# Performance work log

Hardware: AMD Instinct MI355X
Metric: run time of the kernel (lower is better)

Reference implementation:

```python
import jax, jax.numpy as jnp
import numpy as np

D_MODEL = 512
N_HEADS = 8
N_LAYERS = 2
EPS = 1e-5  # torch LayerNorm default


def _ln(x, w, b):
    m = x.mean(-1, keepdims=True)
    v = ((x - m) ** 2).mean(-1, keepdims=True)
    return (x - m) / jnp.sqrt(v + EPS) * w + b


def _mha(q, k, v, in_w, in_b, out_w, out_b, n_heads, mask=None):
    # matches torch.nn.MultiheadAttention (batch_first, packed in_proj of shape (3D, D))
    D = q.shape[-1]
    hd = D // n_heads
    Q = q @ in_w[:D].T + in_b[:D]
    K = k @ in_w[D:2 * D].T + in_b[D:2 * D]
    V = v @ in_w[2 * D:].T + in_b[2 * D:]
    def heads(t):
        B, T, _ = t.shape
        return t.reshape(B, T, n_heads, hd).transpose(0, 2, 1, 3)
    Qh, Kh, Vh = heads(Q), heads(K), heads(V)
    s = jnp.einsum('bhqd,bhkd->bhqk', Qh, Kh) / np.sqrt(hd).astype(np.float32)
    if mask is not None:
        s = s + mask
    a = jax.nn.softmax(s, axis=-1)
    o = jnp.einsum('bhqk,bhkd->bhqd', a, Vh)
    o = o.transpose(0, 2, 1, 3).reshape(q.shape[0], q.shape[1], D)
    return o @ out_w.T + out_b


def _forward(x, ts, ode_w1, ode_b1, ode_w2, ode_b2,
             gru_wih, gru_whh, gru_bih, gru_bhh, te_a, te_b,
             t_in_w, t_in_b, t_out_w, t_out_b, t_ln1_w, t_ln1_b, t_ln2_w, t_ln2_b,
             t_ff1_w, t_ff1_b, t_ff2_w, t_ff2_b, t_lnf_w, t_lnf_b,
             ca_in_w, ca_in_b, ca_out_w, ca_out_b, ca_lin_w, ca_lin_b, ca_ln_w, ca_ln_b):
    B, T, D = x.shape
    # --- RK4 'jump-ODE' states. In the source, h is overwritten with x[:, i] at the
    # end of every step, so state_i depends only on (x[:,i-1], x[:,i], dt_i):
    # fully parallel over T (no scan needed). ODEFunc assumed: MLP tanh.
    ode = lambda y: jnp.tanh(y @ ode_w1.T + ode_b1) @ ode_w2.T + ode_b2
    dt = (ts[:, 1:] - ts[:, :-1])[..., None]            # (B,T-1,1)
    delta = (x[:, 1:] - x[:, :-1]) / dt                  # (B,T-1,D)
    f1 = ode(delta)
    f2 = ode(delta + 0.5 * dt * f1)
    f3 = ode(delta + 0.5 * dt * f2)
    f4 = ode(delta + dt * f3)
    states = x[:, :-1] + dt / 6.0 * (f1 + 2 * f2 + 2 * f3 + f4)
    H = jnp.concatenate([jnp.zeros((B, 1, D), x.dtype), states], axis=1)
    # --- GRUCell recurrence over T (true dependency -> lax.scan)
    Hd = gru_whh.shape[1]
    gx = H @ gru_wih.T + gru_bih                         # (B,T,3H) precomputed input proj
    def gru_step(h, xg):
        gh = h @ gru_whh.T + gru_bhh
        r = jax.nn.sigmoid(xg[:, :Hd] + gh[:, :Hd])
        zz = jax.nn.sigmoid(xg[:, Hd:2 * Hd] + gh[:, Hd:2 * Hd])
        n = jnp.tanh(xg[:, 2 * Hd:] + r * gh[:, 2 * Hd:])
        h = (1 - zz) * n + zz * h
        return h, h
    _, Hs = jax.lax.scan(gru_step, jnp.zeros((B, Hd), x.dtype), gx.transpose(1, 0, 2))
    H = Hs.transpose(1, 0, 2)                            # (B,T,H)
    # --- TimeHybridEncoding: even channels <- interleaved [sin,cos], odd <- ramp
    n_freq = (D // 2) // 2
    freqs = jnp.exp(-jnp.linspace(0.0, np.log(10000.0 / 4.0), n_freq)) * (2.0 * np.pi / 4.0)
    phase = ts[..., None] * freqs                        # (B,T,n_freq)
    sc = jnp.stack([jnp.sin(phase), jnp.cos(phase)], axis=-1).reshape(B, T, -1)
    ramp = ts[..., None] * te_a + te_b                   # (B,T,D//2)
    tm = jnp.zeros((B, T, D), x.dtype).at[..., 0::2].set(sc).at[..., 1::2].set(ramp)
    z = x + tm
    # --- pre-norm TransformerEncoder with causal mask (relu FFN, final LayerNorm)
    mask = jnp.where(jnp.triu(jnp.ones((T, T), bool), 1), jnp.float32(-1e9), jnp.float32(0.0)).astype(x.dtype)
    for l in range(N_LAYERS):
        y = _ln(z, t_ln1_w[l], t_ln1_b[l])
        z = z + _mha(y, y, y, t_in_w[l], t_in_b[l], t_out_w[l], t_out_b[l], N_HEADS, mask)
        y = _ln(z, t_ln2_w[l], t_ln2_b[l])
        z = z + jax.nn.relu(y @ t_ff1_w[l].T + t_ff1_b[l]) @ t_ff2_w[l].T + t_ff2_b[l]
    z = _ln(z, t_lnf_w, t_lnf_b)
    # --- cross attention: query = GRU states, kv = transformer output
    attn = _mha(H, z, z, ca_in_w, ca_in_b, ca_out_w, ca_out_b, N_HEADS, None)
    H = _ln(H + attn @ ca_lin_w.T + ca_lin_b, ca_ln_w, ca_ln_b)
    return H


def setup_inputs() -> dict:
    key = jax.random.key(0)
    B, T, D, L = 8, 1024, D_MODEL, N_LAYERS
    ks = iter(jax.random.split(key, 48))
    nrm = lambda *s: 0.02 * jax.random.normal(next(ks), s, jnp.float32)
    x = jax.random.normal(next(ks), (B, T, D), jnp.float32)
    # strictly increasing, roughly-normalized timestamps
    ts = jnp.cumsum(jax.random.uniform(next(ks), (B, T), jnp.float32, 0.01, 1.0), axis=1) / T
    return dict(
        x=x, ts=ts,
        ode_w1=nrm(D, D), ode_b1=jnp.zeros((D,), jnp.float32),
        ode_w2=nrm(D, D), ode_b2=jnp.zeros((D,), jnp.float32),
        gru_wih=nrm(3 * D, D), gru_whh=nrm(3 * D, D),
        gru_bih=jnp.zeros((3 * D,), jnp.float32), gru_bhh=jnp.zeros((3 * D,), jnp.float32),
        te_a=nrm(D // 2), te_b=nrm(D // 2),
        t_in_w=nrm(L, 3 * D, D), t_in_b=jnp.zeros((L, 3 * D), jnp.float32),
        t_out_w=nrm(L, D, D), t_out_b=jnp.zeros((L, D), jnp.float32),
        t_ln1_w=jnp.ones((L, D), jnp.float32), t_ln1_b=jnp.zeros((L, D), jnp.float32),
        t_ln2_w=jnp.ones((L, D), jnp.float32), t_ln2_b=jnp.zeros((L, D), jnp.float32),
        t_ff1_w=nrm(L, 4 * D, D), t_ff1_b=jnp.zeros((L, 4 * D), jnp.float32),
        t_ff2_w=nrm(L, D, 4 * D), t_ff2_b=jnp.zeros((L, D), jnp.float32),
        t_lnf_w=jnp.ones((D,), jnp.float32), t_lnf_b=jnp.zeros((D,), jnp.float32),
        ca_in_w=nrm(3 * D, D), ca_in_b=jnp.zeros((3 * D,), jnp.float32),
        ca_out_w=nrm(D, D), ca_out_b=jnp.zeros((D,), jnp.float32),
        ca_lin_w=nrm(D, D), ca_lin_b=jnp.zeros((D,), jnp.float32),
        ca_ln_w=jnp.ones((D,), jnp.float32), ca_ln_b=jnp.zeros((D,), jnp.float32))


def reference(x, ts, ode_w1, ode_b1, ode_w2, ode_b2,
              gru_wih, gru_whh, gru_bih, gru_bhh, te_a, te_b,
              t_in_w, t_in_b, t_out_w, t_out_b, t_ln1_w, t_ln1_b, t_ln2_w, t_ln2_b,
              t_ff1_w, t_ff1_b, t_ff2_w, t_ff2_b, t_lnf_w, t_lnf_b,
              ca_in_w, ca_in_b, ca_out_w, ca_out_b, ca_lin_w, ca_lin_b, ca_ln_w, ca_ln_b):
    return _forward(x, ts, ode_w1, ode_b1, ode_w2, ode_b2,
                    gru_wih, gru_whh, gru_bih, gru_bhh, te_a, te_b,
                    t_in_w, t_in_b, t_out_w, t_out_b, t_ln1_w, t_ln1_b, t_ln2_w, t_ln2_b,
                    t_ff1_w, t_ff1_b, t_ff2_w, t_ff2_b, t_lnf_w, t_lnf_b,
                    ca_in_w, ca_in_b, ca_out_w, ca_out_b, ca_lin_w, ca_lin_b, ca_ln_w, ca_ln_b)
```

## Files before the change

### kernel.cpp

```cpp
#include <hip/hip_runtime.h>
#include <math.h>

#define BB 8
#define TT 1024
#define DM 512
#define ROWS (BB*TT)
#define ROWS1 (BB*(TT-1))
#define GRU_J 8
#define GRU_BLK (BB*64)

typedef __attribute__((ext_vector_type(4))) float f32x4;
typedef __attribute__((ext_vector_type(8))) short bf16x8;
typedef __attribute__((ext_vector_type(4))) short bf16x4;

struct RkArgs {
  const float* delta; float* acc; unsigned short* y16;
  const float* dtrow; const int* srcrow;
  const float* x; unsigned short* hin16;
  float wa, cy;
};

__device__ __forceinline__ float sigm_(float v){ return 1.f/(1.f+expf(-v)); }

__device__ __forceinline__ unsigned short f2bf(float f){
  unsigned u = __float_as_uint(f);
  return (unsigned short)((u + 0x7FFFu + ((u>>16)&1u)) >> 16);
}

__global__ __launch_bounds__(256) void castall_kernel(
    const float* w0, const float* w1, const float* w2, const float* w3,
    const float* w4, const float* w5, const float* w6, const float* w7,
    const float* w8, const float* w9, unsigned short* __restrict__ o)
{
  int i = blockIdx.x*256 + threadIdx.x;
  if (i >= 2228224) return;
  const float* src; int off;
  if      (i <   65536){ src=w0; off=0; }
  else if (i <  131072){ src=w1; off=65536; }
  else if (i <  327680){ src=w2; off=131072; }
  else if (i <  720896){ src=w3; off=327680; }
  else if (i <  851968){ src=w4; off=720896; }
  else if (i < 1376256){ src=w5; off=851968; }
  else if (i < 1900544){ src=w6; off=1376256; }
  else if (i < 2097152){ src=w7; off=1900544; }
  else if (i < 2162688){ src=w8; off=2097152; }
  else                 { src=w9; off=2162688; }
  float4 v = ((const float4*)src)[i - off];
  ushort4 u;
  u.x = f2bf(v.x); u.y = f2bf(v.y); u.z = f2bf(v.z); u.w = f2bf(v.w);
  ((ushort4*)o)[i] = u;
}

__global__ __launch_bounds__(256) void delta_kernel(const float* __restrict__ x,
    const float* __restrict__ ts, float* __restrict__ delta,
    unsigned short* __restrict__ delta16,
    float* __restrict__ dtrow, int* __restrict__ srcrow)
{
  size_t i = (size_t)blockIdx.x*256 + threadIdx.x;
  int d = (int)(i & (DM-1));
  int r = (int)(i >> 9);
  int b = r / (TT-1), ii = r % (TT-1);
  float dt = ts[b*TT+ii+1] - ts[b*TT+ii];
  float x1 = x[((size_t)b*TT+ii+1)*DM + d];
  float x0 = x[((size_t)b*TT+ii)*DM + d];
  float v = (x1 - x0) / dt;
  delta[i] = v;
  delta16[i] = f2bf(v);
  if (d == 0) { dtrow[r] = dt; srcrow[r] = b*TT + ii; }
}

__global__ __launch_bounds__(256) void zero8_kernel(unsigned short* __restrict__ hin16)
{
  int tid = threadIdx.x;
  for (int b = 0; b < BB; b++)
    for (int k = tid; k < DM; k += 256)
      hin16[(size_t)b*TT*DM + k] = 0;
}

__global__ __launch_bounds__(256) void timeenc_kernel(const float* __restrict__ x,
    const float* __restrict__ ts, const float* __restrict__ te_a,
    const float* __restrict__ te_b, float* __restrict__ z)
{
  size_t i = (size_t)blockIdx.x*256 + threadIdx.x;
  int d = (int)(i & (DM-1));
  int r = (int)(i >> 9);
  float t = ts[r];
  float tm;
  if (d & 1) {
    int j = d >> 1;
    tm = t*te_a[j] + te_b[j];
  } else {
    int fi = d >> 2;
    float fr = expf(-(float)fi * 0.061606661f) * 1.5707964f;
    float ph = t * fr;
    tm = ((d & 3) == 0) ? sinf(ph) : cosf(ph);
  }
  z[i] = x[i] + tm;
}

template<int BF>
__global__ __launch_bounds__(256) void ln_kernel(const float* __restrict__ x,
    const float* __restrict__ w, const float* __restrict__ b,
    void* __restrict__ outp)
{
  int row = blockIdx.x;
  int tid = threadIdx.x;
  const float* xr = x + (size_t)row*DM;
  float2 v = *(const float2*)(xr + tid*2);
  float s = v.x+v.y, sq = v.x*v.x + v.y*v.y;
  #pragma unroll
  for (int off=1; off<64; off<<=1){ s += __shfl_xor(s,off); sq += __shfl_xor(sq,off); }
  __shared__ float rs[4], rq[4];
  int wid = tid>>6;
  if ((tid&63)==0){ rs[wid]=s; rq[wid]=sq; }
  __syncthreads();
  s = rs[0]+rs[1]+rs[2]+rs[3];
  sq = rq[0]+rq[1]+rq[2]+rq[3];
  float mean = s*(1.f/DM);
  float var = sq*(1.f/DM) - mean*mean;
  float inv = rsqrtf(var + 1e-5f);
  float2 wv = *(const float2*)(w + tid*2);
  float2 bv = *(const float2*)(b + tid*2);
  float ox = (v.x-mean)*inv*wv.x + bv.x;
  float oy = (v.y-mean)*inv*wv.y + bv.y;
  if (BF) {
    ushort2 u; u.x = f2bf(ox); u.y = f2bf(oy);
    *(ushort2*)((unsigned short*)outp + (size_t)row*DM + tid*2) = u;
  } else {
    float2 o; o.x = ox; o.y = oy;
    *(float2*)((float*)outp + (size_t)row*DM + tid*2) = o;
  }
}

template<int ACT, int TN, int RKM>
__global__ __launch_bounds__(256) void bgemm_kernel(
    const unsigned short* __restrict__ A16, const unsigned short* __restrict__ Wb,
    const float* __restrict__ bias, const float* res,
    float* C, unsigned short* Cb, int M, int N, int K, int ldc, RkArgs rk)
{
  const int NJ = TN/32;
  __shared__ __align__(16) unsigned short Al[2][128][40];
  __shared__ __align__(16) unsigned short Wl[2][TN][40];
  const int bm = blockIdx.y*128, bn = blockIdx.x*TN;
  const int tid = threadIdx.x;
  const int lane = tid & 63, wid = tid >> 6;
  const int wm = (wid&1)*64, wn = (wid>>1)*(TN/2);
  const int fl = lane & 15, fk = (lane>>4)*8;
  const int sar = tid>>2, sac = (tid&3)*8;
  f32x4 acc[4][NJ];
  #pragma unroll
  for (int i=0;i<4;i++)
    #pragma unroll
    for (int j=0;j<NJ;j++) acc[i][j] = (f32x4){0.f,0.f,0.f,0.f};

  uint4 areg[2], wreg[TN/64];
  const int nk = K >> 5;

  auto load_t = [&](int kt){
    int k0 = kt*32;
    #pragma unroll
    for (int r=0;r<2;r++){
      int gr = bm + sar + r*64;
      areg[r] = (gr < M) ? *(const uint4*)(A16 + (size_t)gr*K + k0 + sac)
                         : make_uint4(0u,0u,0u,0u);
    }
    #pragma unroll
    for (int r=0;r<TN/64;r++)
      wreg[r] = *(const uint4*)(Wb + (size_t)(bn + sar + r*64)*K + k0 + sac);
  };
  auto store_t = [&](int buf){
    #pragma unroll
    for (int r=0;r<2;r++) *(uint4*)&Al[buf][sar + r*64][sac] = areg[r];
    #pragma unroll
    for (int r=0;r<TN/64;r++) *(uint4*)&Wl[buf][sar + r*64][sac] = wreg[r];
  };

  load_t(0); store_t(0);
  int buf = 0;
  for (int kt = 0; kt < nk; ++kt) {
    __syncthreads();
    if (kt+1 < nk) load_t(kt+1);
    bf16x8 av[4], wv[NJ];
    #pragma unroll
    for (int i=0;i<4;i++) av[i] = *(const bf16x8*)&Al[buf][wm + i*16 + fl][fk];
    #pragma unroll
    for (int j=0;j<NJ;j++) wv[j] = *(const bf16x8*)&Wl[buf][wn + j*16 + fl][fk];
    #pragma unroll
    for (int i=0;i<4;i++)
      #pragma unroll
      for (int j=0;j<NJ;j++)
        acc[i][j] = __builtin_amdgcn_mfma_f32_16x16x32_bf16(av[i], wv[j], acc[i][j], 0, 0, 0);
    if (kt+1 < nk) store_t(buf^1);
    buf ^= 1;
  }

  #pragma unroll
  for (int j=0;j<NJ;j++){
    int gn = bn + wn + j*16 + fl;
    float bv = bias[gn];
    #pragma unroll
    for (int i=0;i<4;i++){
      #pragma unroll
      for (int r=0;r<4;r++){
        int gm = bm + wm + i*16 + (lane>>4)*4 + r;
        if (gm >= M) continue;
        float v = acc[i][j][r] + bv;
        if (ACT==1) v = fmaxf(v, 0.f);
        if (ACT==2) v = tanhf(v);
        if (RKM == 0) {
          if (res) v += res[(size_t)gm*ldc + gn];
          if (C)  C[(size_t)gm*ldc + gn] = v;
          if (Cb) Cb[(size_t)gm*ldc + gn] = f2bf(v);
        } else {
          size_t idx = (size_t)gm*512 + gn;
          float dt = rk.dtrow[gm];
          if (RKM == 1) {
            rk.acc[idx] = v;
            rk.y16[idx] = f2bf(rk.delta[idx] + rk.cy*dt*v);
          } else if (RKM == 2) {
            rk.acc[idx] += rk.wa*v;
            rk.y16[idx] = f2bf(rk.delta[idx] + rk.cy*dt*v);
          } else {
            float a = rk.acc[idx] + v;
            int srow = rk.srcrow[gm];
            rk.hin16[((size_t)srow+1)*512 + gn] =
                f2bf(rk.x[(size_t)srow*512 + gn] + dt*(1.f/6.f)*a);
          }
        }
      }
    }
  }
}

template<int CAUSAL>
__global__ __launch_bounds__(256) void mattn_kernel(
    const unsigned short* __restrict__ QKV, unsigned short* __restrict__ O)
{
  __shared__ __align__(16) unsigned short Kl[32][72];
  __shared__ __align__(16) unsigned short Vt[64][36];
  __shared__ __align__(16) unsigned short Pl[4][16][40];
  const int b = blockIdx.x >> 3, h = blockIdx.x & 7;
  const int q0 = blockIdx.y * 64;
  const int tid = threadIdx.x;
  const int lane = tid & 63, wid = tid >> 6;
  const int lq = lane & 15, g = lane >> 4;
  const size_t rowbase = (size_t)b*TT;

  bf16x8 qf0, qf1;
  {
    const unsigned short* qp = QKV + (rowbase + q0 + wid*16 + lq)*1536 + h*64 + g*8;
    qf0 = *(const bf16x8*)qp;
    qf1 = *(const bf16x8*)(qp + 32);
  }
  f32x4 o[4];
  #pragma unroll
  for (int dt=0; dt<4; dt++) o[dt] = (f32x4){0.f,0.f,0.f,0.f};
  float mr[4] = {-1e30f,-1e30f,-1e30f,-1e30f};
  float Lr[4] = {0.f,0.f,0.f,0.f};

  const int nkt = CAUSAL ? (q0/32 + 2) : (TT/32);
  const int qwmax = q0 + wid*16 + 15;
  const int sr = tid >> 3, scol = (tid & 7) * 8;

  for (int kt = 0; kt < nkt; ++kt) {
    const int k0 = kt*32;
    __syncthreads();
    *(uint4*)&Kl[sr][scol] = *(const uint4*)(QKV + (rowbase + k0 + sr)*1536 + 512 + h*64 + scol);
    {
      uint4 vv = *(const uint4*)(QKV + (rowbase + k0 + sr)*1536 + 1024 + h*64 + scol);
      const unsigned short* vs = (const unsigned short*)&vv;
      #pragma unroll
      for (int i=0;i<8;i++) Vt[scol+i][sr] = vs[i];
    }
    __syncthreads();
    if (CAUSAL && k0 > qwmax) continue;

    f32x4 st0 = (f32x4){0.f,0.f,0.f,0.f}, st1 = (f32x4){0.f,0.f,0.f,0.f};
    {
      bf16x8 kb;
      kb = *(const bf16x8*)&Kl[lq][g*8];
      st0 = __builtin_amdgcn_mfma_f32_16x16x32_bf16(qf0, kb, st0, 0,0,0);
      kb = *(const bf16x8*)&Kl[lq][g*8+32];
      st0 = __builtin_amdgcn_mfma_f32_16x16x32_bf16(qf1, kb, st0, 0,0,0);
      kb = *(const bf16x8*)&Kl[16+lq][g*8];
      st1 = __builtin_amdgcn_mfma_f32_16x16x32_bf16(qf0, kb, st1, 0,0,0);
      kb = *(const bf16x8*)&Kl[16+lq][g*8+32];
      st1 = __builtin_amdgcn_mfma_f32_16x16x32_bf16(qf1, kb, st1, 0,0,0);
    }
    float s0[4], s1[4];
    #pragma unroll
    for (int r=0;r<4;r++){ s0[r] = st0[r]*0.125f; s1[r] = st1[r]*0.125f; }
    if (CAUSAL) {
      int kg0 = k0 + lq, kg1 = k0 + 16 + lq;
      #pragma unroll
      for (int r=0;r<4;r++){
        int qg = q0 + wid*16 + 4*g + r;
        if (kg0 > qg) s0[r] = -1e30f;
        if (kg1 > qg) s1[r] = -1e30f;
      }
    }
    #pragma unroll
    for (int r=0;r<4;r++){
      float v = fmaxf(s0[r], s1[r]);
      v = fmaxf(v, __shfl_xor(v,1));
      v = fmaxf(v, __shfl_xor(v,2));
      v = fmaxf(v, __shfl_xor(v,4));
      v = fmaxf(v, __shfl_xor(v,8));
      float mn = fmaxf(mr[r], v);
      float scl = expf(mr[r] - mn);
      mr[r] = mn;
      float p0 = expf(s0[r] - mn);
      float p1 = expf(s1[r] - mn);
      float lt = p0 + p1;
      lt += __shfl_xor(lt,1); lt += __shfl_xor(lt,2);
      lt += __shfl_xor(lt,4); lt += __shfl_xor(lt,8);
      Lr[r] = Lr[r]*scl + lt;
      o[0][r] *= scl; o[1][r] *= scl; o[2][r] *= scl; o[3][r] *= scl;
      Pl[wid][4*g+r][lq]    = f2bf(p0);
      Pl[wid][4*g+r][16+lq] = f2bf(p1);
    }
    bf16x8 ap = *(const bf16x8*)&Pl[wid][lq][g*8];
    #pragma unroll
    for (int dt=0; dt<4; dt++){
      bf16x4 a4 = *(const bf16x4*)&Vt[lq+16*dt][g*8];
      bf16x4 b4 = *(const bf16x4*)&Vt[lq+16*dt][g*8+4];
      bf16x8 vb = __builtin_shufflevector(a4, b4, 0,1,2,3,4,5,6,7);
      o[dt] = __builtin_amdgcn_mfma_f32_16x16x32_bf16(ap, vb, o[dt], 0,0,0);
    }
  }

  #pragma unroll
  for (int r=0;r<4;r++){
    float inv = 1.f / Lr[r];
    int qg = q0 + wid*16 + 4*g + r;
    unsigned short* op = O + (rowbase + qg)*DM + h*64 + lq;
    op[0]  = f2bf(o[0][r]*inv);
    op[16] = f2bf(o[1][r]*inv);
    op[32] = f2bf(o[2][r]*inv);
    op[48] = f2bf(o[3][r]*inv);
  }
}

__global__ __launch_bounds__(256) void gru_scan_kernel(
    const float* __restrict__ gx,
    const float* __restrict__ whh,
    const float* __restrict__ bhh,
    float* __restrict__ Hs,
    unsigned short* __restrict__ Hsb,
    unsigned long long* hbuf)
{
  __shared__ float wlds[3][GRU_J][512];
  __shared__ float hsp[512];
  const int blk = blockIdx.x;
  const int b = blk & 7;
  const int g = blk >> 3;
  const int j0 = g * GRU_J;
  const int tid = threadIdx.x;

  for (int idx = tid; idx < 3*GRU_J*512/4; idx += 256) {
    int f = idx*4;
    int gate = f >> 12;
    int rem = f & 4095;
    int jj = rem >> 9, k = rem & 511;
    *(float4*)&wlds[gate][jj][k] = *(const float4*)&whh[(size_t)(gate*512 + j0 + jj)*512 + k];
  }
  const int row = tid >> 5;
  const int kl = tid & 31;
  const bool fin = (kl == 0);
  float bh0=0.f, bh1=0.f, bh2=0.f;
  if (fin) { bh0 = bhh[j0+row]; bh1 = bhh[512+j0+row]; bh2 = bhh[1024+j0+row]; }
  __syncthreads();

  for (int t = 0; t < TT; t++) {
    float g0=0.f, g1=0.f, g2=0.f;
    if (fin) {
      const float* gxr = gx + ((size_t)b*TT + t)*1536 + j0 + row;
      g0 = gxr[0]; g1 = gxr[512]; g2 = gxr[1024];
    }
    if (t == 0) {
      hsp[tid] = 0.f; hsp[tid+256] = 0.f;
    } else {
      const unsigned want = (unsigned)t;
      unsigned long long* src = hbuf + ((size_t)((t-1)&1)*BB + b)*512;
      unsigned long long u0, u1;
      for (;;) {
        u0 = __hip_atomic_load(src + tid,       __ATOMIC_RELAXED, __HIP_MEMORY_SCOPE_AGENT);
        u1 = __hip_atomic_load(src + tid + 256, __ATOMIC_RELAXED, __HIP_MEMORY_SCOPE_AGENT);
        if (((unsigned)(u0>>32) == want) & ((unsigned)(u1>>32) == want)) break;
        __builtin_amdgcn_s_sleep(1);
      }
      hsp[tid]     = __uint_as_float((unsigned)u0);
      hsp[tid+256] = __uint_as_float((unsigned)u1);
    }
    __syncthreads();

    float s0=0.f, s1=0.f, s2=0.f;
    #pragma unroll
    for (int j=0;j<4;j++){
      int k = kl*4 + j*128;
      float4 h4 = *(const float4*)&hsp[k];
      float4 a = *(const float4*)&wlds[0][row][k];
      float4 c = *(const float4*)&wlds[1][row][k];
      float4 d = *(const float4*)&wlds[2][row][k];
      s0 += a.x*h4.x + a.y*h4.y + a.z*h4.z + a.w*h4.w;
      s1 += c.x*h4.x + c.y*h4.y + c.z*h4.z + c.w*h4.w;
      s2 += d.x*h4.x + d.y*h4.y + d.z*h4.z + d.w*h4.w;
    }
    #pragma unroll
    for (int off=1; off<32; off<<=1) {
      s0 += __shfl_xor(s0, off);
      s1 += __shfl_xor(s1, off);
      s2 += __shfl_xor(s2, off);
    }
    if (fin) {
      float r  = sigm_(g0 + s0 + bh0);
      float z  = sigm_(g1 + s1 + bh1);
      float n  = tanhf(g2 + r*(s2 + bh2));
      float hold = hsp[j0 + row];
      float hnew = (1.f - z)*n + z*hold;
      size_t off = ((size_t)b*TT + t)*DM + j0 + row;
      Hs[off]  = hnew;
      Hsb[off] = f2bf(hnew);
      unsigned long long pk = ((unsigned long long)(unsigned)(t+1) << 32) | __float_as_uint(hnew);
      __hip_atomic_store(&hbuf[((size_t)(t&1)*BB + b)*512 + j0 + row], pk,
                         __ATOMIC_RELAXED, __HIP_MEMORY_SCOPE_AGENT);
    }
    __syncthreads();
  }
}

static RkArgs g_norm = {};

static void launch_bgemm(int act, int tn, const unsigned short* A16, const unsigned short* Wb,
                         const float* bias, const float* res, float* C, unsigned short* Cb,
                         int M, int N, int K, int ldc, hipStream_t stream)
{
  dim3 blk(256);
  if (tn == 128) {
    dim3 grid(N/128, (M+127)/128);
    switch(act){
      case 1: bgemm_kernel<1,128,0><<<grid,blk,0,stream>>>(A16,Wb,bias,res,C,Cb,M,N,K,ldc,g_norm); break;
      default: bgemm_kernel<0,128,0><<<grid,blk,0,stream>>>(A16,Wb,bias,res,C,Cb,M,N,K,ldc,g_norm); break;
    }
  } else {
    dim3 grid(N/64, (M+127)/128);
    switch(act){
      case 2: bgemm_kernel<2,64,0><<<grid,blk,0,stream>>>(A16,Wb,bias,res,C,Cb,M,N,K,ldc,g_norm); break;
      default: bgemm_kernel<0,64,0><<<grid,blk,0,stream>>>(A16,Wb,bias,res,C,Cb,M,N,K,ldc,g_norm); break;
    }
  }
}

extern "C" void kernel_launch(void* const* d_in, const int* in_sizes, int n_in,
                              void* d_out, int out_size, void* d_ws, size_t ws_size,
                              hipStream_t stream)
{
  (void)in_sizes; (void)n_in; (void)out_size; (void)ws_size;
  const float* x       = (const float*)d_in[0];
  const float* ts      = (const float*)d_in[1];
  const float* ode_w1  = (const float*)d_in[2];
  const float* ode_b1  = (const float*)d_in[3];
  const float* ode_w2  = (const float*)d_in[4];
  const float* ode_b2  = (const float*)d_in[5];
  const float* gru_wih = (const float*)d_in[6];
  const float* gru_whh = (const float*)d_in[7];
  const float* gru_bih = (const float*)d_in[8];
  const float* gru_bhh = (const float*)d_in[9];
  const float* te_a    = (const float*)d_in[10];
  const float* te_b    = (const float*)d_in[11];
  const float* t_in_w  = (const float*)d_in[12];
  const float* t_in_b  = (const float*)d_in[13];
  const float* t_out_w = (const float*)d_in[14];
  const float* t_out_b = (const float*)d_in[15];
  const float* t_ln1_w = (const float*)d_in[16];
  const float* t_ln1_b = (const float*)d_in[17];
  const float* t_ln2_w = (const float*)d_in[18];
  const float* t_ln2_b = (const float*)d_in[19];
  const float* t_ff1_w = (const float*)d_in[20];
  const float* t_ff1_b = (const float*)d_in[21];
  const float* t_ff2_w = (const float*)d_in[22];
  const float* t_ff2_b = (const float*)d_in[23];
  const float* t_lnf_w = (const float*)d_in[24];
  const float* t_lnf_b = (const float*)d_in[25];
  const float* ca_in_w = (const float*)d_in[26];
  const float* ca_in_b = (const float*)d_in[27];
  const float* ca_out_w= (const float*)d_in[28];
  const float* ca_out_b= (const float*)d_in[29];
  const float* ca_lin_w= (const float*)d_in[30];
  const float* ca_lin_b= (const float*)d_in[31];
  const float* ca_ln_w = (const float*)d_in[32];
  const float* ca_ln_b = (const float*)d_in[33];

  float* ws = (float*)d_ws;
  const size_t SZ = (size_t)ROWS * DM;
  float* deltab = ws + 0*SZ;
  float* accb   = ws + 1*SZ;
  float* fcur   = ws + 2*SZ;
  float* gx     = ws + 3*SZ;
  float* zbuf   = ws + 6*SZ;
  float* hsb    = ws + 7*SZ;
  unsigned long long* hbuf = (unsigned long long*)(ws + 8*SZ);
  float* dtrow  = ws + 8*SZ + 16384;
  int*   srcrow = (int*)(ws + 8*SZ + 16384 + 8192);
  unsigned short* u16 = (unsigned short*)(ws + 8*SZ + 16384 + 16384);
  unsigned short* delta16 = u16 + 0*SZ;
  unsigned short* y16     = u16 + 1*SZ;
  unsigned short* t16     = u16 + 2*SZ;
  unsigned short* hs16    = u16 + 3*SZ;
  unsigned short* ff1b16  = u16 + 4*SZ;
  unsigned short* qkv16   = ff1b16;
  unsigned short* ao16    = delta16;
  unsigned short* hin16   = y16;
  unsigned short* cao16   = y16;
  unsigned short* ln16    = t16;
  unsigned short* wb = u16 + 8*SZ;
  unsigned short* wb_ode1 = wb + 0;
  unsigned short* wb_ode2 = wb + 262144;
  unsigned short* wb_gwih = wb + 524288;
  unsigned short* wb_tin  = wb + 1310720;
  unsigned short* wb_tout = wb + 2883584;
  unsigned short* wb_ff1  = wb + 3407872;
  unsigned short* wb_ff2  = wb + 5505024;
  unsigned short* wb_cain = wb + 7602176;
  unsigned short* wb_caout= wb + 8388608;
  unsigned short* wb_calin= wb + 8650752;

  castall_kernel<<<(2228224+255)/256, 256, 0, stream>>>(
      ode_w1, ode_w2, gru_wih, t_in_w, t_out_w, t_ff1_w, t_ff2_w,
      ca_in_w, ca_out_w, ca_lin_w, wb);

  delta_kernel<<<ROWS1*DM/256, 256, 0, stream>>>(x, ts, deltab, delta16, dtrow, srcrow);
  RkArgs rk; rk.delta = deltab; rk.acc = accb; rk.y16 = y16;
  rk.dtrow = dtrow; rk.srcrow = srcrow; rk.x = x; rk.hin16 = hin16;
  const unsigned short* yin16 = delta16;
  const float was[4] = {1.f, 2.f, 2.f, 1.f};
  const float cys[4] = {0.5f, 0.5f, 1.f, 0.f};
  for (int s4 = 0; s4 < 4; s4++) {
    launch_bgemm(2, 64, yin16, wb_ode1, ode_b1, nullptr, nullptr, t16, ROWS1, 512, 512, 512, stream);
    rk.wa = was[s4]; rk.cy = cys[s4];
    dim3 grid(512/64, (ROWS1+127)/128), blk(256);
    if (s4 == 0)
      bgemm_kernel<0,64,1><<<grid,blk,0,stream>>>(t16, wb_ode2, ode_b2, nullptr, nullptr, nullptr, ROWS1, 512, 512, 512, rk);
    else if (s4 < 3)
      bgemm_kernel<0,64,2><<<grid,blk,0,stream>>>(t16, wb_ode2, ode_b2, nullptr, nullptr, nullptr, ROWS1, 512, 512, 512, rk);
    else
      bgemm_kernel<0,64,3><<<grid,blk,0,stream>>>(t16, wb_ode2, ode_b2, nullptr, nullptr, nullptr, ROWS1, 512, 512, 512, rk);
    yin16 = y16;
  }
  zero8_kernel<<<1, 256, 0, stream>>>(hin16);

  launch_bgemm(0, 128, hin16, wb_gwih, gru_bih, nullptr, gx, nullptr, ROWS, 1536, 512, 1536, stream);
  gru_scan_kernel<<<GRU_BLK, 256, 0, stream>>>(gx, gru_whh, gru_bhh, hsb, hs16, hbuf);

  timeenc_kernel<<<ROWS*DM/256,256,0,stream>>>(x, ts, te_a, te_b, zbuf);

  for (int l = 0; l < 2; l++) {
    ln_kernel<1><<<ROWS,256,0,stream>>>(zbuf, t_ln1_w + l*512, t_ln1_b + l*512, ln16);
    launch_bgemm(0, 128, ln16, wb_tin + (size_t)l*1536*512, t_in_b + l*1536, nullptr, nullptr, qkv16, ROWS, 1536, 512, 1536, stream);
    mattn_kernel<1><<<dim3(64, TT/64), 256, 0, stream>>>(qkv16, ao16);
    launch_bgemm(0, 64, ao16, wb_tout + (size_t)l*512*512, t_out_b + l*512, zbuf, zbuf, nullptr, ROWS, 512, 512, 512, stream);
    ln_kernel<1><<<ROWS,256,0,stream>>>(zbuf, t_ln2_w + l*512, t_ln2_b + l*512, ln16);
    launch_bgemm(1, 128, ln16, wb_ff1 + (size_t)l*2048*512, t_ff1_b + l*2048, nullptr, nullptr, ff1b16, ROWS, 2048, 512, 2048, stream);
    launch_bgemm(0, 64, ff1b16, wb_ff2 + (size_t)l*512*2048, t_ff2_b + l*512, zbuf, zbuf, nullptr, ROWS, 512, 2048, 512, stream);
  }
  ln_kernel<1><<<ROWS,256,0,stream>>>(zbuf, t_lnf_w, t_lnf_b, ln16);

  launch_bgemm(0, 64,  hs16, wb_cain,           ca_in_b,       nullptr, nullptr, qkv16,       ROWS,  512, 512, 1536, stream);
  launch_bgemm(0, 128, ln16, wb_cain + 512*512, ca_in_b + 512, nullptr, nullptr, qkv16 + 512, ROWS, 1024, 512, 1536, stream);
  mattn_kernel<0><<<dim3(64, TT/64), 256, 0, stream>>>(qkv16, ao16);
  launch_bgemm(0, 64, ao16, wb_caout, ca_out_b, nullptr, nullptr, cao16, ROWS, 512, 512, 512, stream);
  launch_bgemm(0, 64, cao16, wb_calin, ca_lin_b, hsb, fcur, nullptr, ROWS, 512, 512, 512, stream);
  ln_kernel<0><<<ROWS,256,0,stream>>>(fcur, ca_ln_w, ca_ln_b, (float*)d_out);
}
```

Before: 2.941 ms.

## Use direct global-to-LDS GEMM loads, flag-based GRU sync, fuse time-encoding into LN

The GEMM staging now uses global_load_lds to copy tiles straight into unpadded shared memory, dropping the register round trip and the separate store phase. The GRU scan replaces its spin on packed 64-bit value+step words with per-block step flags polled by one wavefront, followed by plain float loads. Time encoding is fused into the first LayerNorm, and zeroing of the first hidden row moves into the RK4 epilogue, removing two kernel launches. Risks: the unpadded LDS layout can cause bank conflicts, the GEMM drops the M bounds guard, and the flag protocol depends on memory-ordering correctness.

```diff
diff --git a/kernel.cpp b/kernel.cpp
--- a/kernel.cpp
+++ b/kernel.cpp
@@ -12,6 +12,10 @@
 typedef __attribute__((ext_vector_type(4))) float f32x4;
 typedef __attribute__((ext_vector_type(8))) short bf16x8;
 typedef __attribute__((ext_vector_type(4))) short bf16x4;
+
+#define GLOAD16(g, l) __builtin_amdgcn_global_load_lds( \
+    (const __attribute__((address_space(1))) void*)(g), \
+    (__attribute__((address_space(3))) void*)(l), 16, 0, 0)
 
 struct RkArgs {
   const float* delta; float* acc; unsigned short* y16;
@@ -69,44 +73,27 @@
   if (d == 0) { dtrow[r] = dt; srcrow[r] = b*TT + ii; }
 }
 
-__global__ __launch_bounds__(256) void zero8_kernel(unsigned short* __restrict__ hin16)
-{
-  int tid = threadIdx.x;
-  for (int b = 0; b < BB; b++)
-    for (int k = tid; k < DM; k += 256)
-      hin16[(size_t)b*TT*DM + k] = 0;
-}
-
-__global__ __launch_bounds__(256) void timeenc_kernel(const float* __restrict__ x,
-    const float* __restrict__ ts, const float* __restrict__ te_a,
-    const float* __restrict__ te_b, float* __restrict__ z)
-{
-  size_t i = (size_t)blockIdx.x*256 + threadIdx.x;
-  int d = (int)(i & (DM-1));
-  int r = (int)(i >> 9);
-  float t = ts[r];
-  float tm;
-  if (d & 1) {
-    int j = d >> 1;
-    tm = t*te_a[j] + te_b[j];
-  } else {
-    int fi = d >> 2;
-    float fr = expf(-(float)fi * 0.061606661f) * 1.5707964f;
-    float ph = t * fr;
-    tm = ((d & 3) == 0) ? sinf(ph) : cosf(ph);
-  }
-  z[i] = x[i] + tm;
-}
-
-template<int BF>
+template<int BF, int TE>
 __global__ __launch_bounds__(256) void ln_kernel(const float* __restrict__ x,
     const float* __restrict__ w, const float* __restrict__ b,
-    void* __restrict__ outp)
+    void* __restrict__ outp,
+    const float* ts, const float* te_a, const float* te_b, float* zout)
 {
   int row = blockIdx.x;
   int tid = threadIdx.x;
   const float* xr = x + (size_t)row*DM;
   float2 v = *(const float2*)(xr + tid*2);
+  if (TE) {
+    float t = ts[row];
+    int d0 = tid*2;
+    int fi = d0 >> 2;
+    float fr = expf(-(float)fi * 0.061606661f) * 1.5707964f;
+    float ph = t * fr;
+    float tm0 = ((d0 & 3) == 0) ? sinf(ph) : cosf(ph);
+    float tm1 = t*te_a[tid] + te_b[tid];
+    v.x += tm0; v.y += tm1;
+    *(float2*)(zout + (size_t)row*DM + tid*2) = v;
+  }
   float s = v.x+v.y, sq = v.x*v.x + v.y*v.y;
   #pragma unroll
   for (int off=1; off<64; off<<=1){ s += __shfl_xor(s,off); sq += __shfl_xor(sq,off); }
@@ -139,58 +126,60 @@
     float* C, unsigned short* Cb, int M, int N, int K, int ldc, RkArgs rk)
 {
   const int NJ = TN/32;
-  __shared__ __align__(16) unsigned short Al[2][128][40];
-  __shared__ __align__(16) unsigned short Wl[2][TN][40];
+  __shared__ __align__(16) unsigned short Al[2][128*32];
+  __shared__ __align__(16) unsigned short Wl[2][TN*32];
   const int bm = blockIdx.y*128, bn = blockIdx.x*TN;
   const int tid = threadIdx.x;
-  const int lane = tid & 63, wid = tid >> 6;
-  const int wm = (wid&1)*64, wn = (wid>>1)*(TN/2);
+  const int lane = tid & 63, wv = tid >> 6;
+  const int wm = (wv&1)*64, wn = (wv>>1)*(TN/2);
   const int fl = lane & 15, fk = (lane>>4)*8;
-  const int sar = tid>>2, sac = (tid&3)*8;
+  const int srw = lane >> 2;
+  const int scl = (lane & 3)*8;
   f32x4 acc[4][NJ];
   #pragma unroll
   for (int i=0;i<4;i++)
     #pragma unroll
     for (int j=0;j<NJ;j++) acc[i][j] = (f32x4){0.f,0.f,0.f,0.f};
 
-  uint4 areg[2], wreg[TN/64];
   const int nk = K >> 5;
 
-  auto load_t = [&](int kt){
+  auto stage = [&](int buf, int kt){
     int k0 = kt*32;
     #pragma unroll
-    for (int r=0;r<2;r++){
-      int gr = bm + sar + r*64;
-      areg[r] = (gr < M) ? *(const uint4*)(A16 + (size_t)gr*K + k0 + sac)
-                         : make_uint4(0u,0u,0u,0u);
-    }
-    #pragma unroll
-    for (int r=0;r<TN/64;r++)
-      wreg[r] = *(const uint4*)(Wb + (size_t)(bn + sar + r*64)*K + k0 + sac);
+    for (int j=0;j<2;j++){
+      int r = wv*32 + j*16 + srw;
+      GLOAD16(A16 + (size_t)(bm + r)*K + k0 + scl,
+              &Al[buf][(wv*32 + j*16)*32]);
+    }
+    if (TN == 128) {
+      #pragma unroll
+      for (int j=0;j<2;j++){
+        int r = wv*32 + j*16 + srw;
+        GLOAD16(Wb + (size_t)(bn + r)*K + k0 + scl,
+                &Wl[buf][(wv*32 + j*16)*32]);
+      }
+    } else {
+      int r = wv*16 + srw;
+      GLOAD16(Wb + (size_t)(bn + r)*K + k0 + scl,
+              &Wl[buf][(wv*16)*32]);
+    }
   };
-  auto store_t = [&](int buf){
-    #pragma unroll
-    for (int r=0;r<2;r++) *(uint4*)&Al[buf][sar + r*64][sac] = areg[r];
-    #pragma unroll
-    for (int r=0;r<TN/64;r++) *(uint4*)&Wl[buf][sar + r*64][sac] = wreg[r];
-  };
-
-  load_t(0); store_t(0);
+
+  stage(0, 0);
   int buf = 0;
   for (int kt = 0; kt < nk; ++kt) {
     __syncthreads();
-    if (kt+1 < nk) load_t(kt+1);
-    bf16x8 av[4], wv[NJ];
-    #pragma unroll
-    for (int i=0;i<4;i++) av[i] = *(const bf16x8*)&Al[buf][wm + i*16 + fl][fk];
-    #pragma unroll
-    for (int j=0;j<NJ;j++) wv[j] = *(const bf16x8*)&Wl[buf][wn + j*16 + fl][fk];
+    if (kt+1 < nk) stage(buf^1, kt+1);
+    bf16x8 av[4], wvv[NJ];
+    #pragma unroll
+    for (int i=0;i<4;i++) av[i] = *(const bf16x8*)&Al[buf][(wm + i*16 + fl)*32 + fk];
+    #pragma unroll
+    for (int j=0;j<NJ;j++) wvv[j] = *(const bf16x8*)&Wl[buf][(wn + j*16 + fl)*32 + fk];
     #pragma unroll
     for (int i=0;i<4;i++)
       #pragma unroll
       for (int j=0;j<NJ;j++)
-        acc[i][j] = __builtin_amdgcn_mfma_f32_16x16x32_bf16(av[i], wv[j], acc[i][j], 0, 0, 0);
-    if (kt+1 < nk) store_t(buf^1);
+        acc[i][j] = __builtin_amdgcn_mfma_f32_16x16x32_bf16(av[i], wvv[j], acc[i][j], 0, 0, 0);
     buf ^= 1;
   }
 
@@ -225,6 +214,8 @@
             int srow = rk.srcrow[gm];
             rk.hin16[((size_t)srow+1)*512 + gn] =
                 f2bf(rk.x[(size_t)srow*512 + gn] + dt*(1.f/6.f)*a);
+            if ((srow & (TT-1)) == 0)
+              rk.hin16[(size_t)srow*512 + gn] = 0;
           }
         }
       }
@@ -347,7 +338,8 @@
     const float* __restrict__ bhh,
     float* __restrict__ Hs,
     unsigned short* __restrict__ Hsb,
-    unsigned long long* hbuf)
+    float* hbuf,
+    int* flags)
 {
   __shared__ float wlds[3][GRU_J][512];
   __shared__ float hsp[512];
@@ -356,6 +348,7 @@
   const int g = blk >> 3;
   const int j0 = g * GRU_J;
   const int tid = threadIdx.x;
+  const int lane = tid & 63, wv = tid >> 6;
 
   for (int idx = tid; idx < 3*GRU_J*512/4; idx += 256) {
     int f = idx*4;
@@ -380,17 +373,18 @@
     if (t == 0) {
       hsp[tid] = 0.f; hsp[tid+256] = 0.f;
     } else {
-      const unsigned want = (unsigned)t;
-      unsigned long long* src = hbuf + ((size_t)((t-1)&1)*BB + b)*512;
-      unsigned long long u0, u1;
-      for (;;) {
-        u0 = __hip_atomic_load(src + tid,       __ATOMIC_RELAXED, __HIP_MEMORY_SCOPE_AGENT);
-        u1 = __hip_atomic_load(src + tid + 256, __ATOMIC_RELAXED, __HIP_MEMORY_SCOPE_AGENT);
-        if (((unsigned)(u0>>32) == want) & ((unsigned)(u1>>32) == want)) break;
-        __builtin_amdgcn_s_sleep(1);
+      if (wv == 0) {
+        for (;;) {
+          int f = __hip_atomic_load(&flags[b*64 + lane],
+                                    __ATOMIC_RELAXED, __HIP_MEMORY_SCOPE_AGENT);
+          if (__all(f >= t)) break;
+          __builtin_amdgcn_s_sleep(1);
+        }
       }
-      hsp[tid]     = __uint_as_float((unsigned)u0);
-      hsp[tid+256] = __uint_as_float((unsigned)u1);
+      __syncthreads();
+      const float* src = hbuf + (((t-1)&1)*BB + b)*512;
+      hsp[tid]     = __hip_atomic_load(src + tid,       __ATOMIC_RELAXED, __HIP_MEMORY_SCOPE_AGENT);
+      hsp[tid+256] = __hip_atomic_load(src + tid + 256, __ATOMIC_RELAXED, __HIP_MEMORY_SCOPE_AGENT);
     }
     __syncthreads();
 
@@ -412,20 +406,26 @@
       s1 += __shfl_xor(s1, off);
       s2 += __shfl_xor(s2, off);
     }
+    float hnew = 0.f;
     if (fin) {
       float r  = sigm_(g0 + s0 + bh0);
       float z  = sigm_(g1 + s1 + bh1);
       float n  = tanhf(g2 + r*(s2 + bh2));
       float hold = hsp[j0 + row];
-      float hnew = (1.f - z)*n + z*hold;
+      hnew = (1.f - z)*n + z*hold;
+      __hip_atomic_store(&hbuf[((t&1)*BB + b)*512 + j0 + row], hnew,
+                         __ATOMIC_RELAXED, __HIP_MEMORY_SCOPE_AGENT);
+    }
+    asm volatile("s_waitcnt vmcnt(0)" ::: "memory");
+    __syncthreads();
+    if (tid == 0)
+      __hip_atomic_store(&flags[b*64 + g], t+1,
+                         __ATOMIC_RELAXED, __HIP_MEMORY_SCOPE_AGENT);
+    if (fin) {
       size_t off = ((size_t)b*TT + t)*DM + j0 + row;
       Hs[off]  = hnew;
       Hsb[off] = f2bf(hnew);
-      unsigned long long pk = ((unsigned long long)(unsigned)(t+1) << 32) | __float_as_uint(hnew);
-      __hip_atomic_store(&hbuf[((size_t)(t&1)*BB + b)*512 + j0 + row], pk,
-                         __ATOMIC_RELAXED, __HIP_MEMORY_SCOPE_AGENT);
-    }
-    __syncthreads();
+    }
   }
 }
 
@@ -499,7 +499,8 @@
   float* gx     = ws + 3*SZ;
   float* zbuf   = ws + 6*SZ;
   float* hsb    = ws + 7*SZ;
-  unsigned long long* hbuf = (unsigned long long*)(ws + 8*SZ);
+  float* hbuf   = ws + 8*SZ;
+  int*   flags  = (int*)(ws + 8*SZ + 8192);
   float* dtrow  = ws + 8*SZ + 16384;
   int*   srcrow = (int*)(ws + 8*SZ + 16384 + 8192);
   unsigned short* u16 = (unsigned short*)(ws + 8*SZ + 16384 + 16384);
@@ -525,6 +526,7 @@
   unsigned short* wb_caout= wb + 8388608;
   unsigned short* wb_calin= wb + 8650752;
 
+  hipMemsetAsync(flags, 0, GRU_BLK*sizeof(int), stream);
   castall_kernel<<<(2228224+255)/256, 256, 0, stream>>>(
       ode_w1, ode_w2, gru_wih, t_in_w, t_out_w, t_ff1_w, t_ff2_w,
       ca_in_w, ca_out_w, ca_lin_w, wb);
@@ -547,28 +549,32 @@
       bgemm_kernel<0,64,3><<<grid,blk,0,stream>>>(t16, wb_ode2, ode_b2, nullptr, nullptr, nullptr, ROWS1, 512, 512, 512, rk);
     yin16 = y16;
   }
-  zero8_kernel<<<1, 256, 0, stream>>>(hin16);
 
   launch_bgemm(0, 128, hin16, wb_gwih, gru_bih, nullptr, gx, nullptr, ROWS, 1536, 512, 1536, stream);
-  gru_scan_kernel<<<GRU_BLK, 256, 0, stream>>>(gx, gru_whh, gru_bhh, hsb, hs16, hbuf);
-
-  timeenc_kernel<<<ROWS*DM/256,256,0,stream>>>(x, ts, te_a, te_b, zbuf);
+  gru_scan_kernel<<<GRU_BLK, 256, 0, stream>>>(gx, gru_whh, gru_bhh, hsb, hs16, hbuf, flags);
 
   for (int l = 0; l < 2; l++) {
-    ln_kernel<1><<<ROWS,256,0,stream>>>(zbuf, t_ln1_w + l*512, t_ln1_b + l*512, ln16);
+    if (l == 0)
+      ln_kernel<1,1><<<ROWS,256,0,stream>>>(x, t_ln1_w, t_ln1_b, ln16, ts, te_a, te_b, zbuf);
+    else
+      ln_kernel<1,0><<<ROWS,256,0,stream>>>(zbuf, t_ln1_w + 512, t_ln1_b + 512, ln16,
+                                            nullptr, nullptr, nullptr, nullptr);
     launch_bgemm(0, 128, ln16, wb_tin + (size_t)l*1536*512, t_in_b + l*1536, nullptr, nullptr, qkv16, ROWS, 1536, 512, 1536, stream);
     mattn_kernel<1><<<dim3(64, TT/64), 256, 0, stream>>>(qkv16, ao16);
     launch_bgemm(0, 64, ao16, wb_tout + (size_t)l*512*512, t_out_b + l*512, zbuf, zbuf, nullptr, ROWS, 512, 512, 512, stream);
-    ln_kernel<1><<<ROWS,256,0,stream>>>(zbuf, t_ln2_w + l*512, t_ln2_b + l*512, ln16);
+    ln_kernel<1,0><<<ROWS,256,0,stream>>>(zbuf, t_ln2_w + l*512, t_ln2_b + l*512, ln16,
+                                          nullptr, nullptr, nullptr, nullptr);
     launch_bgemm(1, 128, ln16, wb_ff1 + (size_t)l*2048*512, t_ff1_b + l*2048, nullptr, nullptr, ff1b16, ROWS, 2048, 512, 2048, stream);
     launch_bgemm(0, 64, ff1b16, wb_ff2 + (size_t)l*512*2048, t_ff2_b + l*512, zbuf, zbuf, nullptr, ROWS, 512, 2048, 512, stream);
   }
-  ln_kernel<1><<<ROWS,256,0,stream>>>(zbuf, t_lnf_w, t_lnf_b, ln16);
+  ln_kernel<1,0><<<ROWS,256,0,stream>>>(zbuf, t_lnf_w, t_lnf_b, ln16,
+                                        nullptr, nullptr, nullptr, nullptr);
 
   launch_bgemm(0, 64,  hs16, wb_cain,           ca_in_b,       nullptr, nullptr, qkv16,       ROWS,  512, 512, 1536, stream);
   launch_bgemm(0, 128, ln16, wb_cain + 512*512, ca_in_b + 512, nullptr, nullptr, qkv16 + 512, ROWS, 1024, 512, 1536, stream);
   mattn_kernel<0><<<dim3(64, TT/64), 256, 0, stream>>>(qkv16, ao16);
   launch_bgemm(0, 64, ao16, wb_caout, ca_out_b, nullptr, nullptr, cao16, ROWS, 512, 512, 512, stream);
   launch_bgemm(0, 64, cao16, wb_calin, ca_lin_b, hsb, fcur, nullptr, ROWS, 512, 512, 512, stream);
-  ln_kernel<0><<<ROWS,256,0,stream>>>(fcur, ca_ln_w, ca_ln_b, (float*)d_out);
-}
+  ln_kernel<0,0><<<ROWS,256,0,stream>>>(fcur, ca_ln_w, ca_ln_b, (float*)d_out,
+                                        nullptr, nullptr, nullptr, nullptr);
+}
```

New measurement: 6.377 ms. +116.8%, slower.
